# Optimization experiments

Measured on AMD Instinct MI355X. Metric: run time of the kernel, lower is better.

## Reference

```python
import jax, jax.numpy as jnp
import numpy as np

B, T, I = 32, 512, 64      # batch, seq_len, input_size
F, H = 64, 64              # num_filterbanks, hidden_size


def setup_inputs() -> dict:
    key = jax.random.key(0)
    k1, k2 = jax.random.split(key)
    x = jax.random.normal(k1, (B, T, I), dtype=jnp.float32)
    # torch.nn.Linear weight has shape (out_features=F, in_features=I)
    W = jax.random.normal(k2, (F, I), dtype=jnp.float32) / np.sqrt(I)
    relax = jnp.full((F,), 0.5, dtype=jnp.float32)
    return {"input": x, "W": W, "relax": relax}


def reference(input, W, relax):
    x = input                                  # (B, T, I)
    sq = jnp.sqrt(relax)                       # (F,) sqrt(relax)
    gain = jnp.sqrt(1.0 - relax)               # sqrt(1 - sqrt(relax)^2) = sqrt(1-relax)

    # Hoist the per-step input projection: input_block(input).t() for all t.
    u = jnp.einsum('bti,fi->tfb', x, W)        # (T, F, B)
    h0 = jnp.zeros((F, x.shape[0], H), x.dtype)

    def time_step(h, u_t):
        # h: (F, B, H) previous hiddens; u_t: (F, B)
        b0 = sq[:, None] * h[..., 0] + gain[:, None] * u_t          # (F, B)
        # inner recurrence over hidden index i:
        #   h_new[i] = sq*h_new[i-1] + (sq*h[i] - h[i-1])
        c = sq[:, None, None] * h[..., 1:] - h[..., :-1]            # (F, B, H-1)

        def inner(prev, c_i):
            new = sq[:, None] * prev + c_i
            return new, new

        _, ys = jax.lax.scan(inner, b0, jnp.moveaxis(c, -1, 0))     # (H-1, F, B)
        h_new = jnp.concatenate([b0[..., None], jnp.moveaxis(ys, 0, -1)], axis=-1)  # (F,B,H)
        return h_new, h_new

    h_final, hs = jax.lax.scan(time_step, h0, u)   # hs: (T, F, B, H)
    output = jnp.transpose(hs, (2, 0, 1, 3))       # (B, T, F, H)
    return output, h_final
```

## Files before the change

kernel.cpp:

```cpp
#include <hip/hip_runtime.h>
#include <math.h>

#define TT 512
#define FF 64
#define BB 32
#define HH 64
#define NSLOT 96
#define RSF 64

__device__ __forceinline__ float shift_up1(float v, int j16) {
    int s1 = __builtin_amdgcn_update_dpp(0, __float_as_int(v), 0x111, 0xf, 0xf, true);
    int s2 = __builtin_amdgcn_update_dpp(0, __float_as_int(v), 0x142, 0xf, 0xf, false);
    return __int_as_float((j16 == 0) ? s2 : s1);
}

#define STEP(MASKED, UK) do {                                          \
    const float shifted_ = shift_up1(vlast, j16);                      \
    const float nbr_cur_ = isj0 ? (UK) : shifted_;                     \
    float v_ = fmaf(cA, nbr_cur_, fmaf(a, prev, -nbr_prev));           \
    if (MASKED) {                                                      \
        const bool live_ = ((unsigned)t < (unsigned)TT);               \
        v_ = live_ ? v_ : prev;                                        \
        if (live_) *(float*)((char*)ring + vaddr) = v_;                \
    } else {                                                           \
        *(float*)((char*)ring + vaddr) = v_;                           \
    }                                                                  \
    vaddr += 256; vaddr = (vaddr == vtop) ? vbase : vaddr;             \
    nbr_prev = isj0 ? 0.f : nbr_cur_;                                  \
    prev = v_; vlast = v_;                                             \
    ++t;                                                               \
} while (0)

#define READS(G0, G1, G2, G3, OPP) do {                                \
    const float* rp_ = ring + (sb + (l >> 4)) * RSF + (j16 << 2);      \
    G0 = *(const float4*)(rp_ + 0 * 4 * RSF);                          \
    G1 = *(const float4*)(rp_ + 1 * 4 * RSF);                          \
    G2 = *(const float4*)(rp_ + 2 * 4 * RSF);                          \
    G3 = *(const float4*)(rp_ + 3 * 4 * RSF);                          \
    OPP = ochunk + ((size_t)(l >> 4) << 12) + (j16 << 2);              \
    ochunk += 16 * 4096;                                               \
    sb += 16; if (sb == NSLOT) sb = 0;                                 \
} while (0)

#define STORES(G0, G1, G2, G3, OPP) do {                               \
    *(float4*)(OPP + (size_t)0 * 16384) = G0;                          \
    *(float4*)(OPP + (size_t)1 * 16384) = G1;                          \
    *(float4*)(OPP + (size_t)2 * 16384) = G2;                          \
    *(float4*)(OPP + (size_t)3 * 16384) = G3;                          \
} while (0)

#define PT_RD_A do { READS(gA0,gA1,gA2,gA3, opA); } while (0)
#define PT_AB   do { STORES(gA0,gA1,gA2,gA3, opA); READS(gB0,gB1,gB2,gB3, opB); } while (0)
#define PT_BA   do { STORES(gB0,gB1,gB2,gB3, opB); READS(gA0,gA1,gA2,gA3, opA); } while (0)
#define NOPT    do {} while (0)

#define HALF(UREG, HS, MASKED, P6, P22) do {                           \
    _Pragma("unroll")                                                  \
    for (int i_ = 0; i_ < 32; ++i_) {                                  \
        const float uk_ = __int_as_float(                              \
            __builtin_amdgcn_readlane(__float_as_int(UREG), (HS) * 32 + i_)); \
        STEP(MASKED, uk_);                                             \
        if (i_ == 6)  { P6; }                                          \
        if (i_ == 22) { P22; }                                         \
    }                                                                  \
} while (0)

#define PAIR_STEADY(UREG) do {                                         \
    HALF(UREG, 0, false, PT_AB, PT_BA);                                \
    HALF(UREG, 1, false, PT_AB, PT_BA);                                \
} while (0)

__global__ __launch_bounds__(64) void lru_kernel(
    const float* __restrict__ x,
    const float* __restrict__ W,
    const float* __restrict__ relax,
    float* __restrict__ out)
{
    __shared__ float ring[NSLOT * RSF];

    const int w = blockIdx.x;
    const int b = w >> 6;
    const int f = w & 63;
    const int l = threadIdx.x;
    const int j16 = l & 15;

    float ua[8];
    {
        const float4* __restrict__ Wv = reinterpret_cast<const float4*>(W) + (size_t)f * 16;
        float4 wreg[16];
        #pragma unroll
        for (int q = 0; q < 16; ++q) wreg[q] = Wv[q];
        const float4* __restrict__ xb = reinterpret_cast<const float4*>(x) + (size_t)b * TT * 16;
        #pragma unroll
        for (int c = 0; c < 8; ++c) {
            const int tt = (c << 6) + l;
            const float4* xv = xb + (size_t)tt * 16;
            float acc = 0.f;
            #pragma unroll
            for (int q = 0; q < 16; ++q) {
                const float4 xq = xv[q], wq = wreg[q];
                acc = fmaf(xq.x, wq.x, fmaf(xq.y, wq.y, fmaf(xq.z, wq.z, fmaf(xq.w, wq.w, acc))));
            }
            ua[c] = acc;
        }
    }

    const float rel = relax[f];
    const float a  = sqrtf(rel);
    const float gn = sqrtf(1.0f - rel);
    const bool isj0 = (l == 0);
    const float cA = isj0 ? gn : a;

    float prev = 0.f, nbr_prev = 0.f, vlast = 0.f;
    int t = -l;

    const int vbase = l << 2;
    const int vtop  = NSLOT * 256 + vbase;
    int vaddr = ((NSLOT - l) % NSLOT) * 256 + vbase;

    int sb = 0;
    float* ochunk = out + (size_t)b * (TT * FF * HH) + (size_t)f * HH;
    float4 gA0, gA1, gA2, gA3, gB0, gB1, gB2, gB3;
    float *opA = nullptr, *opB = nullptr;

    HALF(ua[0], 0, true, NOPT, NOPT);
    HALF(ua[0], 1, true, NOPT, NOPT);

    HALF(ua[1], 0, false, NOPT, PT_RD_A);
    HALF(ua[1], 1, false, PT_AB, PT_BA);

    PAIR_STEADY(ua[2]);
    PAIR_STEADY(ua[3]);
    PAIR_STEADY(ua[4]);
    PAIR_STEADY(ua[5]);
    PAIR_STEADY(ua[6]);
    PAIR_STEADY(ua[7]);

    HALF(ua[7], 0, true, PT_AB, PT_BA);
    HALF(ua[7], 1, true, PT_AB, PT_BA);

    STORES(gA0, gA1, gA2, gA3, opA);
    READS(gB0, gB1, gB2, gB3, opB);
    STORES(gB0, gB1, gB2, gB3, opB);

    out[(size_t)BB * TT * FF * HH + ((size_t)f * BB + b) * HH + l] = prev;
}

extern "C" void kernel_launch(void* const* d_in, const int* in_sizes, int n_in,
                              void* d_out, int out_size, void* d_ws, size_t ws_size,
                              hipStream_t stream) {
    const float* x     = (const float*)d_in[0];
    const float* W     = (const float*)d_in[1];
    const float* relax = (const float*)d_in[2];
    float* out = (float*)d_out;
    lru_kernel<<<dim3(2048), dim3(64), 0, stream>>>(x, W, relax, out);
}
```

Baseline: 81.60 us.

## Split recurrence into checkpoint pass and time-chunked parallel recompute pass

The single wavefront-per-chain kernel becomes two kernels. The first runs the full wavefront recurrence without writing the large output, saving the projected inputs and hidden-state checkpoints every 64 timesteps to workspace. The second launches 512 blocks, one per batch, time-chunk and filter half. Each block recomputes 64 timesteps from a checkpoint, with each lane handling 8 hidden units, and streams the outputs through a shared-memory ring to global memory. This spreads the output writes over more parallel work and shortens the serial store path, at the cost of redundant recurrence work, workspace traffic and an extra launch; the old kernel remains as a fallback when the workspace is too small.

```diff
diff --git a/kernel.cpp b/kernel.cpp
--- a/kernel.cpp
+++ b/kernel.cpp
@@ -5,18 +5,224 @@
 #define FF 64
 #define BB 32
 #define HH 64
-#define NSLOT 96
-#define RSF 64
 
 __device__ __forceinline__ float shift_up1(float v, int j16) {
     int s1 = __builtin_amdgcn_update_dpp(0, __float_as_int(v), 0x111, 0xf, 0xf, true);
     int s2 = __builtin_amdgcn_update_dpp(0, __float_as_int(v), 0x142, 0xf, 0xf, false);
     return __int_as_float((j16 == 0) ? s2 : s1);
 }
-
-#define STEP(MASKED, UK) do {                                          \
+__device__ __forceinline__ float dpp_row_shr1(float v) {
+    int r = __builtin_amdgcn_update_dpp(0, __float_as_int(v), 0x111, 0xf, 0xf, true);
+    return __int_as_float(r);
+}
+
+#define P1STEP(K) do {                                                  \
+    const int ci_ = ((K) >> 6) > 7 ? 7 : ((K) >> 6);                    \
+    const float uk_ = __int_as_float(__builtin_amdgcn_readlane(         \
+        __float_as_int(ua[ci_]), (K) & 63));                            \
+    const float shifted_ = shift_up1(vlast, j16);                       \
+    const float nbr_cur_ = isl0 ? uk_ : shifted_;                       \
+    float v_ = fmaf(cA, nbr_cur_, fmaf(a, prev, -nbr_prev));            \
+    const bool live_ = ((unsigned)t < (unsigned)TT);                    \
+    v_ = live_ ? v_ : prev;                                             \
+    if ((K) >= 63 && (K) <= 510) {                                      \
+        const int cc_ = ((K) + 1) >> 6;                                 \
+        if (l == (K) - (cc_ << 6) + 1) ck[cc_ - 1] = v_;                \
+    }                                                                   \
+    nbr_prev = isl0 ? 0.f : nbr_cur_;                                   \
+    prev = v_; vlast = v_;                                              \
+    ++t;                                                                \
+} while (0)
+
+#define P1HALF(BASE) do {                                               \
+    _Pragma("unroll")                                                   \
+    for (int i_ = 0; i_ < 32; ++i_) { P1STEP((BASE) + i_); }            \
+} while (0)
+
+__global__ __launch_bounds__(64) void lru_pass1(
+    const float* __restrict__ x,
+    const float* __restrict__ W,
+    const float* __restrict__ relax,
+    float* __restrict__ out,
+    float* __restrict__ ws_u,
+    float* __restrict__ ws_ck)
+{
+    const int w = blockIdx.x;
+    const int b = w >> 6;
+    const int f = w & 63;
+    const int l = threadIdx.x;
+    const int j16 = l & 15;
+
+    float ua[8];
+    {
+        const float4* __restrict__ Wv = reinterpret_cast<const float4*>(W) + (size_t)f * 16;
+        float4 wreg[16];
+        #pragma unroll
+        for (int q = 0; q < 16; ++q) wreg[q] = Wv[q];
+        const float4* __restrict__ xb = reinterpret_cast<const float4*>(x) + (size_t)b * TT * 16;
+        #pragma unroll
+        for (int c = 0; c < 8; ++c) {
+            const int tt = (c << 6) + l;
+            const float4* xv = xb + (size_t)tt * 16;
+            float acc = 0.f;
+            #pragma unroll
+            for (int q = 0; q < 16; ++q) {
+                const float4 xq = xv[q], wq = wreg[q];
+                acc = fmaf(xq.x, wq.x, fmaf(xq.y, wq.y, fmaf(xq.z, wq.z, fmaf(xq.w, wq.w, acc))));
+            }
+            ua[c] = acc;
+        }
+    }
+
+    const float rel = relax[f];
+    const float a  = sqrtf(rel);
+    const float gn = sqrtf(1.0f - rel);
+    const bool isl0 = (l == 0);
+    const float cA = isl0 ? gn : a;
+
+    float prev = 0.f, nbr_prev = 0.f, vlast = 0.f;
+    float ck[7];
+    int t = -l;
+
+    P1HALF(0);   P1HALF(32);  P1HALF(64);  P1HALF(96);
+    P1HALF(128); P1HALF(160); P1HALF(192); P1HALF(224);
+    P1HALF(256); P1HALF(288); P1HALF(320); P1HALF(352);
+    P1HALF(384); P1HALF(416); P1HALF(448); P1HALF(480);
+    P1HALF(512); P1HALF(544);
+
+    const size_t chain = (size_t)b * 64 + f;
+    float* uw = ws_u + chain * 512;
+    #pragma unroll
+    for (int c = 0; c < 8; ++c) uw[(c << 6) + l] = ua[c];
+    float* cw = ws_ck + chain * 512;
+    cw[l] = 0.f;
+    #pragma unroll
+    for (int c = 1; c < 8; ++c) cw[(c << 6) + l] = ck[c - 1];
+
+    out[(size_t)BB * TT * FF * HH + ((size_t)f * BB + b) * HH + l] = prev;
+}
+
+__global__ __launch_bounds__(256) void lru_pass2(
+    const float* __restrict__ ws_u,
+    const float* __restrict__ ws_ck,
+    const float* __restrict__ relax,
+    float* __restrict__ out)
+{
+    __shared__ float ring[16 * 2048];
+    __shared__ float u2[32 * 68];
+
+    const int bid = blockIdx.x;
+    const int tc = bid & 7;
+    const int fg = (bid >> 3) & 1;
+    const int b  = bid >> 4;
+    const int t0 = tc << 6;
+    const int f0 = fg << 5;
+    const int tid  = threadIdx.x;
+    const int wv   = tid >> 6;
+    const int lane = tid & 63;
+    const int g = lane >> 3;
+    const int j = lane & 7;
+    const int fl = (wv << 3) | g;
+    const size_t chain = (size_t)b * 64 + f0 + fl;
+
+    #pragma unroll
+    for (int q = 0; q < 2; ++q) {
+        const int idx  = (q << 8) + tid;
+        const int flr  = idx >> 4;
+        const int part = idx & 15;
+        const float4 v = *(const float4*)(ws_u + ((size_t)b * 64 + f0 + flr) * 512
+                                               + t0 + (part << 2));
+        *(float4*)(u2 + flr * 68 + (part << 2)) = v;
+    }
+
+    const float rel = relax[f0 + fl];
+    const float a  = sqrtf(rel);
+    const float gn = sqrtf(1.0f - rel);
+    const bool isj0 = (j == 0);
+    const float cA = isj0 ? gn : a;
+
+    const float* sp = ws_ck + chain * 512 + (tc << 6) + (j << 3);
+    const float4 s0 = *(const float4*)(sp);
+    const float4 s1 = *(const float4*)(sp + 4);
+    float p0 = s0.x, p1 = s0.y, p2 = s0.z, p3 = s0.w;
+    float p4 = s1.x, p5 = s1.y, p6 = s1.z, p7 = s1.w;
+    float vlast = p7;
+    float nbr_prev = 0.f;
+
+    const int uoff  = fl * 68;
+    const int vbase = (fl << 8) + (j << 5);
+    const int vtop  = (16 << 13) + vbase;
+    int vaddr = (((16 - j) & 15) << 13) + vbase;
+
+    __syncthreads();
+
+    int k = 0;
+    for (int s = 0; s < 18; ++s) {
+        #pragma unroll
+        for (int ii = 0; ii < 4; ++ii) {
+            const int tt = k - j;
+            const float uk = u2[uoff + (k & 63)];
+            const float shifted = dpp_row_shr1(vlast);
+            const float nbr_cur = isj0 ? uk : shifted;
+            float n0 = fmaf(cA, nbr_cur, fmaf(a, p0, -nbr_prev));
+            float n1 = fmaf(a, n0, fmaf(a, p1, -p0));
+            float n2 = fmaf(a, n1, fmaf(a, p2, -p1));
+            float n3 = fmaf(a, n2, fmaf(a, p3, -p2));
+            float n4 = fmaf(a, n3, fmaf(a, p4, -p3));
+            float n5 = fmaf(a, n4, fmaf(a, p5, -p4));
+            float n6 = fmaf(a, n5, fmaf(a, p6, -p5));
+            float n7 = fmaf(a, n6, fmaf(a, p7, -p6));
+            const bool live = ((unsigned)tt < 64u);
+            n0 = live ? n0 : p0;  n1 = live ? n1 : p1;
+            n2 = live ? n2 : p2;  n3 = live ? n3 : p3;
+            n4 = live ? n4 : p4;  n5 = live ? n5 : p5;
+            n6 = live ? n6 : p6;  n7 = live ? n7 : p7;
+            if (live) {
+                float4 w0; w0.x = n0; w0.y = n1; w0.z = n2; w0.w = n3;
+                float4 w1; w1.x = n4; w1.y = n5; w1.z = n6; w1.w = n7;
+                *(float4*)((char*)ring + vaddr)      = w0;
+                *(float4*)((char*)ring + vaddr + 16) = w1;
+            }
+            vaddr += 8192; vaddr = (vaddr == vtop) ? vbase : vaddr;
+            nbr_prev = isj0 ? 0.f : nbr_cur;
+            p0 = n0; p1 = n1; p2 = n2; p3 = n3;
+            p4 = n4; p5 = n5; p6 = n6; p7 = n7;
+            vlast = n7;
+            ++k;
+        }
+        __syncthreads();
+        if (s >= 2) {
+            const int rr = ((s << 2) - 8) + wv;
+            const float* rp = ring + ((rr & 15) << 11) + (lane << 2);
+            float* op = out + (((size_t)((b << 9) + t0 + rr)) << 12)
+                            + (fg << 11) + (lane << 2);
+            float4 q0 = *(const float4*)(rp + 0 * 256);
+            float4 q1 = *(const float4*)(rp + 1 * 256);
+            float4 q2 = *(const float4*)(rp + 2 * 256);
+            float4 q3 = *(const float4*)(rp + 3 * 256);
+            float4 q4 = *(const float4*)(rp + 4 * 256);
+            float4 q5 = *(const float4*)(rp + 5 * 256);
+            float4 q6 = *(const float4*)(rp + 6 * 256);
+            float4 q7 = *(const float4*)(rp + 7 * 256);
+            *(float4*)(op + 0 * 256) = q0;
+            *(float4*)(op + 1 * 256) = q1;
+            *(float4*)(op + 2 * 256) = q2;
+            *(float4*)(op + 3 * 256) = q3;
+            *(float4*)(op + 4 * 256) = q4;
+            *(float4*)(op + 5 * 256) = q5;
+            *(float4*)(op + 6 * 256) = q6;
+            *(float4*)(op + 7 * 256) = q7;
+        }
+    }
+}
+
+#define NSLOT 96
+#define RSF 64
+#define STEP(MASKED) do {                                              \
+    const float uk_ = __int_as_float(__builtin_amdgcn_readlane(        \
+        __float_as_int(UREG_), LIDX_));                                \
     const float shifted_ = shift_up1(vlast, j16);                      \
-    const float nbr_cur_ = isj0 ? (UK) : shifted_;                     \
+    const float nbr_cur_ = isj0 ? uk_ : shifted_;                      \
     float v_ = fmaf(cA, nbr_cur_, fmaf(a, prev, -nbr_prev));           \
     if (MASKED) {                                                      \
         const bool live_ = ((unsigned)t < (unsigned)TT);               \
@@ -30,7 +236,6 @@
     prev = v_; vlast = v_;                                             \
     ++t;                                                               \
 } while (0)
-
 #define READS(G0, G1, G2, G3, OPP) do {                                \
     const float* rp_ = ring + (sb + (l >> 4)) * RSF + (j16 << 2);      \
     G0 = *(const float4*)(rp_ + 0 * 4 * RSF);                          \
@@ -41,49 +246,41 @@
     ochunk += 16 * 4096;                                               \
     sb += 16; if (sb == NSLOT) sb = 0;                                 \
 } while (0)
-
 #define STORES(G0, G1, G2, G3, OPP) do {                               \
     *(float4*)(OPP + (size_t)0 * 16384) = G0;                          \
     *(float4*)(OPP + (size_t)1 * 16384) = G1;                          \
     *(float4*)(OPP + (size_t)2 * 16384) = G2;                          \
     *(float4*)(OPP + (size_t)3 * 16384) = G3;                          \
 } while (0)
-
 #define PT_RD_A do { READS(gA0,gA1,gA2,gA3, opA); } while (0)
 #define PT_AB   do { STORES(gA0,gA1,gA2,gA3, opA); READS(gB0,gB1,gB2,gB3, opB); } while (0)
 #define PT_BA   do { STORES(gB0,gB1,gB2,gB3, opB); READS(gA0,gA1,gA2,gA3, opA); } while (0)
 #define NOPT    do {} while (0)
-
 #define HALF(UREG, HS, MASKED, P6, P22) do {                           \
+    const float UREG_ = (UREG);                                        \
     _Pragma("unroll")                                                  \
     for (int i_ = 0; i_ < 32; ++i_) {                                  \
-        const float uk_ = __int_as_float(                              \
-            __builtin_amdgcn_readlane(__float_as_int(UREG), (HS) * 32 + i_)); \
-        STEP(MASKED, uk_);                                             \
+        const int LIDX_ = (HS) * 32 + i_;                              \
+        STEP(MASKED);                                                  \
         if (i_ == 6)  { P6; }                                          \
         if (i_ == 22) { P22; }                                         \
     }                                                                  \
 } while (0)
-
 #define PAIR_STEADY(UREG) do {                                         \
     HALF(UREG, 0, false, PT_AB, PT_BA);                                \
     HALF(UREG, 1, false, PT_AB, PT_BA);                                \
 } while (0)
 
-__global__ __launch_bounds__(64) void lru_kernel(
-    const float* __restrict__ x,
-    const float* __restrict__ W,
-    const float* __restrict__ relax,
-    float* __restrict__ out)
+__global__ __launch_bounds__(64) void lru_fallback(
+    const float* __restrict__ x, const float* __restrict__ W,
+    const float* __restrict__ relax, float* __restrict__ out)
 {
     __shared__ float ring[NSLOT * RSF];
-
     const int w = blockIdx.x;
     const int b = w >> 6;
     const int f = w & 63;
     const int l = threadIdx.x;
     const int j16 = l & 15;
-
     float ua[8];
     {
         const float4* __restrict__ Wv = reinterpret_cast<const float4*>(W) + (size_t)f * 16;
@@ -104,45 +301,35 @@
             ua[c] = acc;
         }
     }
-
     const float rel = relax[f];
     const float a  = sqrtf(rel);
     const float gn = sqrtf(1.0f - rel);
     const bool isj0 = (l == 0);
     const float cA = isj0 ? gn : a;
-
     float prev = 0.f, nbr_prev = 0.f, vlast = 0.f;
     int t = -l;
-
     const int vbase = l << 2;
     const int vtop  = NSLOT * 256 + vbase;
     int vaddr = ((NSLOT - l) % NSLOT) * 256 + vbase;
-
     int sb = 0;
     float* ochunk = out + (size_t)b * (TT * FF * HH) + (size_t)f * HH;
     float4 gA0, gA1, gA2, gA3, gB0, gB1, gB2, gB3;
     float *opA = nullptr, *opB = nullptr;
-
     HALF(ua[0], 0, true, NOPT, NOPT);
     HALF(ua[0], 1, true, NOPT, NOPT);
-
     HALF(ua[1], 0, false, NOPT, PT_RD_A);
     HALF(ua[1], 1, false, PT_AB, PT_BA);
-
     PAIR_STEADY(ua[2]);
     PAIR_STEADY(ua[3]);
     PAIR_STEADY(ua[4]);
     PAIR_STEADY(ua[5]);
     PAIR_STEADY(ua[6]);
     PAIR_STEADY(ua[7]);
-
     HALF(ua[7], 0, true, PT_AB, PT_BA);
     HALF(ua[7], 1, true, PT_AB, PT_BA);
-
     STORES(gA0, gA1, gA2, gA3, opA);
     READS(gB0, gB1, gB2, gB3, opB);
     STORES(gB0, gB1, gB2, gB3, opB);
-
     out[(size_t)BB * TT * FF * HH + ((size_t)f * BB + b) * HH + l] = prev;
 }
 
@@ -153,5 +340,13 @@
     const float* W     = (const float*)d_in[1];
     const float* relax = (const float*)d_in[2];
     float* out = (float*)d_out;
-    lru_kernel<<<dim3(2048), dim3(64), 0, stream>>>(x, W, relax, out);
-}
+    const size_t need = (size_t)2048 * 512 * 4 * 2;
+    if (ws_size >= need) {
+        float* ws_u  = (float*)d_ws;
+        float* ws_ck = ws_u + (size_t)2048 * 512;
+        lru_pass1<<<dim3(2048), dim3(64), 0, stream>>>(x, W, relax, out, ws_u, ws_ck);
+        lru_pass2<<<dim3(512), dim3(256), 0, stream>>>(ws_u, ws_ck, relax, out);
+    } else {
+        lru_fallback<<<dim3(2048), dim3(64), 0, stream>>>(x, W, relax, out);
+    }
+}
```

Measured after the change: 114.9 us. 40.9% more time.

## Split LRU into checkpoint pass and parallel chunked recompute-and-write pass

Applied to the files above, without the earlier changes.

The first pass still runs the wavefront recurrence, but it only saves hidden-state checkpoints every 16 timesteps plus the input projection to workspace instead of writing the full output. A second kernel launches 1024 blocks, one per (batch, 16-step chunk), that recompute the recurrence from those checkpoints and write the outputs through an LDS transpose, so the bulk output writes happen in parallel. This takes the large output store traffic off the serial critical path, at the cost of a second launch, extra workspace traffic and duplicated arithmetic. The original kernel stays as a fallback when the workspace is too small.

```diff
diff --git a/kernel.cpp b/kernel.cpp
--- a/kernel.cpp
+++ b/kernel.cpp
@@ -5,8 +5,6 @@
 #define FF 64
 #define BB 32
 #define HH 64
-#define NSLOT 96
-#define RSF 64
 
 __device__ __forceinline__ float shift_up1(float v, int j16) {
     int s1 = __builtin_amdgcn_update_dpp(0, __float_as_int(v), 0x111, 0xf, 0xf, true);
@@ -14,6 +12,174 @@
     return __int_as_float((j16 == 0) ? s2 : s1);
 }
 
+#define P1STEP(K, MASKED, UK) do {                                     \
+    const float shifted_ = shift_up1(vlast, j16);                      \
+    const float nbr_cur_ = isl0 ? (UK) : shifted_;                     \
+    float v_ = fmaf(cA, nbr_cur_, fmaf(a, prev, -nbr_prev));           \
+    if (MASKED) {                                                      \
+        const bool live_ = ((unsigned)t < (unsigned)TT);               \
+        v_ = live_ ? v_ : prev;                                        \
+    }                                                                  \
+    if ((K) >= 15 && (K) <= 558) {                                     \
+        bool cap_ = (j16 == (((K) + 1) & 15));                         \
+        if ((K) < 79)  cap_ = cap_ && (l <= (K) - 15);                 \
+        if ((K) > 495) cap_ = cap_ && (l >= (K) - 495);                \
+        if (cap_) ckl[(((K) + 1) >> 4) * 4096] = v_;                   \
+    }                                                                  \
+    nbr_prev = isl0 ? 0.f : nbr_cur_;                                  \
+    prev = v_; vlast = v_;                                             \
+    ++t;                                                               \
+} while (0)
+
+#define P1HALF(BASE, UREG, MASKED) do {                                \
+    _Pragma("unroll")                                                  \
+    for (int i_ = 0; i_ < 32; ++i_) {                                  \
+        const float uk_ = __int_as_float(__builtin_amdgcn_readlane(    \
+            __float_as_int(UREG), (((BASE) & 63) + i_)));              \
+        P1STEP((BASE) + i_, MASKED, uk_);                              \
+    }                                                                  \
+} while (0)
+
+__global__ __launch_bounds__(64) void lru_pass1(
+    const float* __restrict__ x,
+    const float* __restrict__ W,
+    const float* __restrict__ relax,
+    float* __restrict__ out,
+    float* __restrict__ ws_u,
+    float* __restrict__ ws_ck)
+{
+    const int w = blockIdx.x;
+    const int b = w >> 6;
+    const int f = w & 63;
+    const int l = threadIdx.x;
+    const int j16 = l & 15;
+
+    float ua[8];
+    {
+        const float4* __restrict__ Wv = reinterpret_cast<const float4*>(W) + (size_t)f * 16;
+        float4 wreg[16];
+        #pragma unroll
+        for (int q = 0; q < 16; ++q) wreg[q] = Wv[q];
+        const float4* __restrict__ xb = reinterpret_cast<const float4*>(x) + (size_t)b * TT * 16;
+        #pragma unroll
+        for (int c = 0; c < 8; ++c) {
+            const int tt = (c << 6) + l;
+            const float4* xv = xb + (size_t)tt * 16;
+            float acc = 0.f;
+            #pragma unroll
+            for (int q = 0; q < 16; ++q) {
+                const float4 xq = xv[q], wq = wreg[q];
+                acc = fmaf(xq.x, wq.x, fmaf(xq.y, wq.y, fmaf(xq.z, wq.z, fmaf(xq.w, wq.w, acc))));
+            }
+            ua[c] = acc;
+        }
+    }
+
+    {
+        float* uw = ws_u + (size_t)b * (TT * FF) + (size_t)l * FF + f;
+        #pragma unroll
+        for (int c = 0; c < 8; ++c) uw[(size_t)c * 64 * FF] = ua[c];
+    }
+
+    const float rel = relax[f];
+    const float a  = sqrtf(rel);
+    const float gn = sqrtf(1.0f - rel);
+    const bool isl0 = (l == 0);
+    const float cA = isl0 ? gn : a;
+
+    float prev = 0.f, nbr_prev = 0.f, vlast = 0.f;
+    int t = -l;
+    float* ckl = ws_ck + (size_t)b * 131072 + (size_t)f * 64 + l - ((size_t)(l >> 4)) * 4096;
+
+    P1HALF(0,   ua[0], true);  P1HALF(32,  ua[0], true);
+    P1HALF(64,  ua[1], false); P1HALF(96,  ua[1], false);
+    P1HALF(128, ua[2], false); P1HALF(160, ua[2], false);
+    P1HALF(192, ua[3], false); P1HALF(224, ua[3], false);
+    P1HALF(256, ua[4], false); P1HALF(288, ua[4], false);
+    P1HALF(320, ua[5], false); P1HALF(352, ua[5], false);
+    P1HALF(384, ua[6], false); P1HALF(416, ua[6], false);
+    P1HALF(448, ua[7], false); P1HALF(480, ua[7], false);
+    P1HALF(512, ua[7], true);  P1HALF(544, ua[7], true);
+
+    out[(size_t)BB * TT * FF * HH + ((size_t)f * BB + b) * HH + l] = prev;
+}
+
+__global__ __launch_bounds__(64) void lru_pass2(
+    const float* __restrict__ ws_u,
+    const float* __restrict__ ws_ck,
+    const float* __restrict__ relax,
+    float* __restrict__ out)
+{
+    __shared__ float buf[2][4096];
+
+    const int bid = blockIdx.x;
+    const int b = bid >> 5;
+    const int c = bid & 31;
+    const int f = threadIdx.x;
+
+    const float rel = relax[f];
+    const float a  = sqrtf(rel);
+    const float gn = sqrtf(1.0f - rel);
+
+    float h[64];
+    if (c == 0) {
+        #pragma unroll
+        for (int i = 0; i < 64; ++i) h[i] = 0.f;
+    } else {
+        const float4* sp = reinterpret_cast<const float4*>(
+            ws_ck + (size_t)b * 131072 + (size_t)c * 4096 + (size_t)f * 64);
+        #pragma unroll
+        for (int m = 0; m < 16; ++m) {
+            const float4 v = sp[m];
+            h[4*m] = v.x; h[4*m+1] = v.y; h[4*m+2] = v.z; h[4*m+3] = v.w;
+        }
+    }
+
+    float uu[16];
+    {
+        const float* up = ws_u + (size_t)b * (TT * FF) + (size_t)(c * 16) * FF + f;
+        #pragma unroll
+        for (int r = 0; r < 16; ++r) uu[r] = up[(size_t)r * FF];
+    }
+
+    char* rowOut = (char*)(out + ((size_t)b * TT + (size_t)c * 16) * (FF * HH));
+
+    #pragma unroll
+    for (int r = 0; r < 16; ++r) {
+        float prev_new = fmaf(gn, uu[r], fmaf(a, h[0], -0.0f));
+        float old_im1 = h[0];
+        h[0] = prev_new;
+        #pragma unroll
+        for (int i = 1; i < 64; ++i) {
+            const float nw = fmaf(a, prev_new, fmaf(a, h[i], -old_im1));
+            old_im1 = h[i];
+            h[i] = nw;
+            prev_new = nw;
+        }
+        {
+            char* bp = (char*)buf[r & 1];
+            #pragma unroll
+            for (int m = 0; m < 16; ++m) {
+                float4 v; v.x = h[4*m]; v.y = h[4*m+1]; v.z = h[4*m+2]; v.w = h[4*m+3];
+                *(float4*)(bp + f * 256 + (((m + f) & 15) << 4)) = v;
+            }
+        }
+        {
+            const char* bp = (const char*)buf[r & 1];
+            #pragma unroll
+            for (int i = 0; i < 16; ++i) {
+                const int fr = i * 4 + (f >> 4);
+                const int cr = f & 15;
+                const float4 q = *(const float4*)(bp + fr * 256 + (((cr + fr) & 15) << 4));
+                *(float4*)(rowOut + i * 1024 + f * 16) = q;
+            }
+        }
+        rowOut += 16384;
+    }
+}
+
+#define NSLOT 96
+#define RSF 64
 #define STEP(MASKED, UK) do {                                          \
     const float shifted_ = shift_up1(vlast, j16);                      \
     const float nbr_cur_ = isj0 ? (UK) : shifted_;                     \
@@ -30,7 +196,6 @@
     prev = v_; vlast = v_;                                             \
     ++t;                                                               \
 } while (0)
-
 #define READS(G0, G1, G2, G3, OPP) do {                                \
     const float* rp_ = ring + (sb + (l >> 4)) * RSF + (j16 << 2);      \
     G0 = *(const float4*)(rp_ + 0 * 4 * RSF);                          \
@@ -41,19 +206,16 @@
     ochunk += 16 * 4096;                                               \
     sb += 16; if (sb == NSLOT) sb = 0;                                 \
 } while (0)
-
 #define STORES(G0, G1, G2, G3, OPP) do {                               \
     *(float4*)(OPP + (size_t)0 * 16384) = G0;                          \
     *(float4*)(OPP + (size_t)1 * 16384) = G1;                          \
     *(float4*)(OPP + (size_t)2 * 16384) = G2;                          \
     *(float4*)(OPP + (size_t)3 * 16384) = G3;                          \
 } while (0)
-
 #define PT_RD_A do { READS(gA0,gA1,gA2,gA3, opA); } while (0)
 #define PT_AB   do { STORES(gA0,gA1,gA2,gA3, opA); READS(gB0,gB1,gB2,gB3, opB); } while (0)
 #define PT_BA   do { STORES(gB0,gB1,gB2,gB3, opB); READS(gA0,gA1,gA2,gA3, opA); } while (0)
 #define NOPT    do {} while (0)
-
 #define HALF(UREG, HS, MASKED, P6, P22) do {                           \
     _Pragma("unroll")                                                  \
     for (int i_ = 0; i_ < 32; ++i_) {                                  \
@@ -64,26 +226,21 @@
         if (i_ == 22) { P22; }                                         \
     }                                                                  \
 } while (0)
-
 #define PAIR_STEADY(UREG) do {                                         \
     HALF(UREG, 0, false, PT_AB, PT_BA);                                \
     HALF(UREG, 1, false, PT_AB, PT_BA);                                \
 } while (0)
 
-__global__ __launch_bounds__(64) void lru_kernel(
-    const float* __restrict__ x,
-    const float* __restrict__ W,
-    const float* __restrict__ relax,
-    float* __restrict__ out)
+__global__ __launch_bounds__(64) void lru_fallback(
+    const float* __restrict__ x, const float* __restrict__ W,
+    const float* __restrict__ relax, float* __restrict__ out)
 {
     __shared__ float ring[NSLOT * RSF];
-
     const int w = blockIdx.x;
     const int b = w >> 6;
     const int f = w & 63;
     const int l = threadIdx.x;
     const int j16 = l & 15;
-
     float ua[8];
     {
         const float4* __restrict__ Wv = reinterpret_cast<const float4*>(W) + (size_t)f * 16;
@@ -104,45 +261,35 @@
             ua[c] = acc;
         }
     }
-
     const float rel = relax[f];
     const float a  = sqrtf(rel);
     const float gn = sqrtf(1.0f - rel);
     const bool isj0 = (l == 0);
     const float cA = isj0 ? gn : a;
-
     float prev = 0.f, nbr_prev = 0.f, vlast = 0.f;
     int t = -l;
-
     const int vbase = l << 2;
     const int vtop  = NSLOT * 256 + vbase;
     int vaddr = ((NSLOT - l) % NSLOT) * 256 + vbase;
-
     int sb = 0;
     float* ochunk = out + (size_t)b * (TT * FF * HH) + (size_t)f * HH;
     float4 gA0, gA1, gA2, gA3, gB0, gB1, gB2, gB3;
     float *opA = nullptr, *opB = nullptr;
-
     HALF(ua[0], 0, true, NOPT, NOPT);
     HALF(ua[0], 1, true, NOPT, NOPT);
-
     HALF(ua[1], 0, false, NOPT, PT_RD_A);
     HALF(ua[1], 1, false, PT_AB, PT_BA);
-
     PAIR_STEADY(ua[2]);
     PAIR_STEADY(ua[3]);
     PAIR_STEADY(ua[4]);
     PAIR_STEADY(ua[5]);
     PAIR_STEADY(ua[6]);
     PAIR_STEADY(ua[7]);
-
     HALF(ua[7], 0, true, PT_AB, PT_BA);
     HALF(ua[7], 1, true, PT_AB, PT_BA);
-
     STORES(gA0, gA1, gA2, gA3, opA);
     READS(gB0, gB1, gB2, gB3, opB);
     STORES(gB0, gB1, gB2, gB3, opB);
-
     out[(size_t)BB * TT * FF * HH + ((size_t)f * BB + b) * HH + l] = prev;
 }
 
@@ -153,5 +300,13 @@
     const float* W     = (const float*)d_in[1];
     const float* relax = (const float*)d_in[2];
     float* out = (float*)d_out;
-    lru_kernel<<<dim3(2048), dim3(64), 0, stream>>>(x, W, relax, out);
-}
+    const size_t need = ((size_t)BB * TT * FF + (size_t)BB * 32 * FF * HH) * 4;
+    if (ws_size >= need) {
+        float* ws_u  = (float*)d_ws;
+        float* ws_ck = ws_u + (size_t)BB * TT * FF;
+        lru_pass1<<<dim3(2048), dim3(64), 0, stream>>>(x, W, relax, out, ws_u, ws_ck);
+        lru_pass2<<<dim3(1024), dim3(64), 0, stream>>>(ws_u, ws_ck, relax, out);
+    } else {
+        lru_fallback<<<dim3(2048), dim3(64), 0, stream>>>(x, W, relax, out);
+    }
+}
```

Result: slower. 123.4 us (+51.2%).
